# Kernel optimization log

Measured on AMD Instinct MI355X. Metric: run time of the kernel, lower is better.

Reference implementation:

```python
import jax, jax.numpy as jnp
import numpy as np

HID, STEM, BN_OUT, STEM_OUT, MLP = 256, 64, 128, 64, 128
BN_WS, STEM_WS = 5, 17
N, H_BN, W_BN, H_VIS, W_VIS = 4096, 128, 128, 1024, 1024


def setup_inputs() -> dict:
    key = jax.random.key(0)
    ks = jax.random.split(key, 24)
    f32 = jnp.float32
    def rn(k, shape, s=0.05):
        return jax.random.normal(k, shape, f32) * s
    return dict(
        bottleneck=rn(ks[0], (1, HID, H_BN, W_BN), 1.0),
        vis_stem_features=rn(ks[1], (1, STEM, H_VIS, W_VIS), 1.0),
        source_positions_vis=jax.random.uniform(ks[2], (N, 2), f32, 10.0, W_VIS - 10.0),
        pixel_to_sky=rn(ks[3], (N, 2, 2), 0.1),
        fused_h=H_BN, fused_w=W_BN, vis_h=H_VIS, vis_w=W_VIS,
        dw_w=rn(ks[4], (HID, 1, 7, 7)), dw_b=rn(ks[5], (HID,)),
        ln_g=jnp.ones((HID,), f32), ln_b=jnp.zeros((HID,), f32),
        pw1_w=rn(ks[6], (4 * HID, HID)), pw1_b=rn(ks[7], (4 * HID,)),
        pw2_w=rn(ks[8], (HID, 4 * HID)), pw2_b=rn(ks[9], (HID,)),
        cn_gamma=jnp.full((HID,), 1e-2, f32),
        bn1x1_w=rn(ks[10], (BN_OUT, HID, 1, 1)), bn1x1_b=rn(ks[11], (BN_OUT,)),
        st1_w=rn(ks[12], (STEM_OUT, STEM, 3, 3)), st1_b=rn(ks[13], (STEM_OUT,)),
        st2_w=rn(ks[14], (STEM_OUT, STEM_OUT, 3, 3)), st2_b=rn(ks[15], (STEM_OUT,)),
        h1_w=rn(ks[16], (MLP, BN_OUT + STEM_OUT)), h1_b=rn(ks[17], (MLP,)),
        h2_w=rn(ks[18], (MLP, MLP)), h2_b=rn(ks[19], (MLP,)),
        h3_w=rn(ks[20], (3, MLP)),
        h3_b=jnp.array([0.0, 0.0, float(np.log(0.05))], f32),
    )


def _gelu(x):
    return jax.nn.gelu(x, approximate=False)


def _conv2d(x, w, b, padding, groups=1):
    y = jax.lax.conv_general_dilated(
        x, w, (1, 1), [(padding, padding), (padding, padding)],
        dimension_numbers=('NCHW', 'OIHW', 'NCHW'), feature_group_count=groups)
    return y + b[None, :, None, None]


def _bilinear_windows(fm, pos, ws):
    """fm [1,C,H,W], pos [N,2] pixel coords -> [N,C,ws,ws].
    Matches torch grid_sample(mode=bilinear, padding=zeros, align_corners=True)
    with the module's normalize/unnormalize, i.e. direct pixel-coord sampling."""
    C, H, W = fm.shape[1:]
    fm2 = fm[0]
    half = ws // 2
    off = jnp.arange(-half, half + 1, dtype=pos.dtype)
    gy, gx = jnp.meshgrid(off, off, indexing='ij')
    xs = gx[None] + pos[:, 0, None, None]   # [N,ws,ws]
    ys = gy[None] + pos[:, 1, None, None]
    x0 = jnp.floor(xs); y0 = jnp.floor(ys)
    wx1 = xs - x0; wy1 = ys - y0
    x0i = x0.astype(jnp.int32); y0i = y0.astype(jnp.int32)
    def gather(yi, xi, w):
        valid = (yi >= 0) & (yi < H) & (xi >= 0) & (xi < W)
        v = fm2[:, jnp.clip(yi, 0, H - 1), jnp.clip(xi, 0, W - 1)]  # [C,N,ws,ws]
        return v * (w * valid)[None]
    out = (gather(y0i, x0i, (1 - wy1) * (1 - wx1))
           + gather(y0i, x0i + 1, (1 - wy1) * wx1)
           + gather(y0i + 1, x0i, wy1 * (1 - wx1))
           + gather(y0i + 1, x0i + 1, wy1 * wx1))
    return jnp.transpose(out, (1, 0, 2, 3))


def _gauss(ws):
    t = jnp.linspace(-1.0, 1.0, ws)
    yy, xx = jnp.meshgrid(t, t, indexing='ij')
    g = jnp.exp(-(xx ** 2 + yy ** 2) / (2 * 0.4 ** 2))
    return g / g.sum()


def _convnext(x, dw_w, dw_b, ln_g, ln_b, pw1_w, pw1_b, pw2_w, pw2_b, gamma):
    r = x
    x = _conv2d(x, dw_w, dw_b, padding=3, groups=x.shape[1])  # depthwise 7x7
    mu = x.mean(1, keepdims=True)
    var = ((x - mu) ** 2).mean(1, keepdims=True)
    x = (x - mu) / jnp.sqrt(var + 1e-6)
    x = x * ln_g[None, :, None, None] + ln_b[None, :, None, None]
    x = jnp.einsum('nchw,oc->nohw', x, pw1_w) + pw1_b[None, :, None, None]
    x = _gelu(x)
    x = jnp.einsum('nchw,oc->nohw', x, pw2_w) + pw2_b[None, :, None, None]
    return r + gamma[None, :, None, None] * x


def _forward(bottleneck, vis_stem_features, source_positions_vis, pixel_to_sky,
             dw_w, dw_b, ln_g, ln_b, pw1_w, pw1_b, pw2_w, pw2_b, cn_gamma,
             bn1x1_w, bn1x1_b, st1_w, st1_b, st2_w, st2_b,
             h1_w, h1_b, h2_w, h2_b, h3_w, h3_b,
             fused_h, fused_w, vis_h, vis_w):
    scale = jnp.array([fused_w / vis_w, fused_h / vis_h], source_positions_vis.dtype)
    pos_bn = source_positions_vis * scale
    # bottleneck branch: 5x5 windows -> ConvNeXt -> 1x1 conv -> GELU -> gauss pool
    bn_win = _bilinear_windows(bottleneck, pos_bn, BN_WS)              # [N,256,5,5]
    bn_feat = _convnext(bn_win, dw_w, dw_b, ln_g, ln_b, pw1_w, pw1_b, pw2_w, pw2_b, cn_gamma)
    bn_feat = _gelu(_conv2d(bn_feat, bn1x1_w, bn1x1_b, padding=0))     # [N,128,5,5]
    bn_vec = (bn_feat * _gauss(BN_WS)[None, None]).sum((-2, -1))       # [N,128]
    st_win = _bilinear_windows(vis_stem_features, source_positions_vis, STEM_WS)
    st = _gelu(_conv2d(st_win, st1_w, st1_b, padding=1))
    st = _gelu(_conv2d(st, st2_w, st2_b, padding=1))                   # [N,64,17,17]
    st_vec = (st * _gauss(STEM_WS)[None, None]).sum((-2, -1))          # [N,64]
    # head MLP
    x = jnp.concatenate([bn_vec, st_vec], axis=1)                      # [N,192]
    x = _gelu(x @ h1_w.T + h1_b)
    x = _gelu(x @ h2_w.T + h2_b)
    out = x @ h3_w.T + h3_b                                            # [N,3]
    dx_px, dy_px = out[:, 0], out[:, 1]
    log_sigma = jnp.clip(out[:, 2], -6.0, 3.0)
    pix = jnp.stack([dx_px, dy_px], axis=1)                            # [N,2]
    pred_sky = jnp.einsum('nij,nj->ni', pixel_to_sky, pix)             # [N,2]
    confidence = 1.0 / jnp.maximum(jnp.exp(log_sigma), 1e-4)
    return pred_sky, dx_px, dy_px, log_sigma, confidence


def reference(bottleneck, vis_stem_features, source_positions_vis, pixel_to_sky,
              fused_h, fused_w, vis_h, vis_w,
              dw_w, dw_b, ln_g, ln_b, pw1_w, pw1_b, pw2_w, pw2_b, cn_gamma,
              bn1x1_w, bn1x1_b, st1_w, st1_b, st2_w, st2_b,
              h1_w, h1_b, h2_w, h2_b, h3_w, h3_b):
    return _forward(bottleneck, vis_stem_features, source_positions_vis, pixel_to_sky,
                    dw_w, dw_b, ln_g, ln_b, pw1_w, pw1_b, pw2_w, pw2_b, cn_gamma,
                    bn1x1_w, bn1x1_b, st1_w, st1_b, st2_w, st2_b,
                    h1_w, h1_b, h2_w, h2_b, h3_w, h3_b,
                    fused_h, fused_w, vis_h, vis_w)
```

## Files before the change

kernel.cpp:

```cpp
#include <hip/hip_runtime.h>
#include <hip/hip_bf16.h>

#define XSTR 28

typedef short short8 __attribute__((ext_vector_type(8)));
typedef float f32x4  __attribute__((ext_vector_type(4)));
typedef float f32x16 __attribute__((ext_vector_type(16)));

__device__ __forceinline__ float gelu_f(float x){
    return 0.5f*x*(1.0f + erff(x*0.70710678118654752f));
}
__device__ __forceinline__ float gelu_q(float x){
    const float z = 1.5957691216057308f*x*(1.0f + 0.044715f*x*x);
    return x / (1.0f + __expf(-z));
}
__device__ __forceinline__ unsigned short f2bf(float f){
    unsigned int u = __float_as_uint(f);
    u += 0x7fffu + ((u>>16)&1u);
    return (unsigned short)(u>>16);
}
__device__ __forceinline__ unsigned int pack2(float a, float b){
    return (unsigned int)f2bf(a) | ((unsigned int)f2bf(b)<<16);
}
__device__ __forceinline__ float bf_lo(unsigned int u){ return __uint_as_float(u<<16); }
__device__ __forceinline__ float bf_hi(unsigned int u){ return __uint_as_float(u & 0xffff0000u); }
__device__ __forceinline__ float bfu(unsigned short v){ return __uint_as_float(((unsigned int)v)<<16); }

__device__ __forceinline__ void fma_row25(const float* __restrict__ row, float w, float* __restrict__ acc){
    const float4* r4 = (const float4*)row;
    float4 a0=r4[0], a1=r4[1], a2=r4[2], a3=r4[3], a4=r4[4], a5=r4[5];
    float a6 = row[24];
    acc[0]+=a0.x*w;  acc[1]+=a0.y*w;  acc[2]+=a0.z*w;  acc[3]+=a0.w*w;
    acc[4]+=a1.x*w;  acc[5]+=a1.y*w;  acc[6]+=a1.z*w;  acc[7]+=a1.w*w;
    acc[8]+=a2.x*w;  acc[9]+=a2.y*w;  acc[10]+=a2.z*w; acc[11]+=a2.w*w;
    acc[12]+=a3.x*w; acc[13]+=a3.y*w; acc[14]+=a3.z*w; acc[15]+=a3.w*w;
    acc[16]+=a4.x*w; acc[17]+=a4.y*w; acc[18]+=a4.z*w; acc[19]+=a4.w*w;
    acc[20]+=a5.x*w; acc[21]+=a5.y*w; acc[22]+=a5.z*w; acc[23]+=a5.w*w;
    acc[24]+=a6*w;
}

__device__ __forceinline__ void bn_body(
    unsigned char* __restrict__ U, int n0, int t,
    const float* __restrict__ bottleneck, const float* __restrict__ pos,
    const float* __restrict__ dw_w, const float* __restrict__ dw_b,
    const float* __restrict__ ln_g, const float* __restrict__ ln_b,
    const float* __restrict__ pw1_b, const float* __restrict__ pw2_b,
    const float* __restrict__ cn_gamma, const float* __restrict__ bn1x1_b,
    const short8* __restrict__ P1v, const short8* __restrict__ P2v,
    const short8* __restrict__ Pbv,
    float* __restrict__ vec_out)
{
    unsigned char* Xb = U;
    unsigned char* Hc = U + 32768;
    float* redA = (float*)(U + 49152);
    float* redB = (float*)(U + 50752);
    float* muS  = (float*)(U + 52352);
    float* rsS  = (float*)(U + 52576);

    const int lane = t & 63, w = t >> 6;
    const int mcol = lane & 15, h4 = lane >> 4;
    const int sP = t >> 8, cP = t & 255;

    unsigned int wvp[13];
    float xdw[25];
    {
        const int n = n0 + sP;
        const float px = pos[2*n]*0.125f, py = pos[2*n+1]*0.125f;
        const float fpx = floorf(px), fpy = floorf(py);
        const int ix0 = (int)fpx - 2, iy0 = (int)fpy - 2;
        const float fx = px - fpx, fy = py - fpy;
        const float w00=(1.f-fy)*(1.f-fx), w01=(1.f-fy)*fx, w10=fy*(1.f-fx), w11=fy*fx;
        float wv[25];
        {
            const float* fm = bottleneck + cP*16384;
            float P[6][6];
            #pragma unroll
            for (int r=0;r<6;r++){
                const int y = iy0+r;
                const bool yok = (y>=0)&&(y<128);
                const int yc = y<0?0:(y>127?127:y);
                #pragma unroll
                for (int s=0;s<6;s++){
                    const int x = ix0+s;
                    const bool ok = yok && (x>=0) && (x<128);
                    const int xc = x<0?0:(x>127?127:x);
                    P[r][s] = ok ? fm[yc*128+xc] : 0.f;
                }
            }
            #pragma unroll
            for (int a=0;a<5;a++)
            #pragma unroll
            for (int b=0;b<5;b++)
                wv[a*5+b] = w00*P[a][b]+w01*P[a][b+1]+w10*P[a+1][b]+w11*P[a+1][b+1];
        }
        #pragma unroll
        for (int i=0;i<12;i++) wvp[i] = pack2(wv[2*i], wv[2*i+1]);
        wvp[12] = pack2(wv[24], 0.f);
        {
            float wcr[49];
            const float* wc = dw_w + cP*49;
            #pragma unroll
            for (int k=0;k<49;k++) wcr[k]=wc[k];
            const float bb = dw_b[cP];
            #pragma unroll
            for (int i=0;i<5;i++){
                #pragma unroll
                for (int j=0;j<5;j++){
                    float a = bb;
                    #pragma unroll
                    for (int u=0;u<7;u++){
                        const int y = i+u-3;
                        if (y<0||y>4) continue;
                        #pragma unroll
                        for (int v=0;v<7;v++){
                            const int x = j+v-3;
                            if (x<0||x>4) continue;
                            a += wv[y*5+x]*wcr[u*7+v];
                        }
                    }
                    xdw[i*5+j] = a;
                }
            }
        }
        #pragma unroll
        for (int p=0;p<25;p++){
            const int row = sP*32 + p;
            *(unsigned short*)(Xb + row*512 + ((2*cP) ^ ((row&7)<<4))) = f2bf(xdw[p]);
        }
    }
    __syncthreads();
    if (t < 400){
        const int sp = t>>3, part = t&7;
        const int row = (sp/25)*32 + (sp - (sp/25)*25);
        float a=0.f, b=0.f;
        for (int c=part; c<256; c+=8){
            const float v = bfu(*(const unsigned short*)(Xb + row*512 + ((2*c) ^ ((row&7)<<4))));
            a += v; b += v*v;
        }
        redA[t]=a; redB[t]=b;
    }
    __syncthreads();
    if (t < 50){
        float a=0.f, b=0.f;
        #pragma unroll
        for (int s=0;s<8;s++){ a+=redA[t*8+s]; b+=redB[t*8+s]; }
        const float m = a*(1.f/256.f);
        const float var = b*(1.f/256.f) - m*m;
        muS[t]=m; rsS[t]=rsqrtf(var+1e-6f);
    }
    __syncthreads();
    {
        const float g = ln_g[cP], bb = ln_b[cP];
        #pragma unroll
        for (int p=0;p<25;p++){
            const int row = sP*32 + p;
            const float v = (xdw[p]-muS[sP*25+p])*rsS[sP*25+p]*g + bb;
            *(unsigned short*)(Xb + row*512 + ((2*cP) ^ ((row&7)<<4))) = f2bf(v);
        }
    }
    __syncthreads();

    f32x4 acc2[2][4];
    #pragma unroll
    for (int ml=0;ml<2;ml++)
        #pragma unroll
        for (int nt=0;nt<4;nt++) acc2[ml][nt]=0.f;

    for (int ch=0; ch<8; ++ch){
        const int mt = ch*8 + w;
        f32x4 a1[4];
        #pragma unroll
        for (int nt=0;nt<4;nt++) a1[nt]=0.f;
        #pragma unroll
        for (int kk=0; kk<8; ++kk){
            const short8 av = P1v[((mt<<3)+kk)*64 + lane];
            #pragma unroll
            for (int nt=0; nt<4; ++nt){
                const int row = nt*16 + mcol;
                const int ad = row*512 + ((kk*64 + h4*16) ^ ((row&7)<<4));
                const short8 bv = *(const short8*)(Xb + ad);
                a1[nt] = __builtin_amdgcn_mfma_f32_16x16x32_bf16(av, bv, a1[nt], 0,0,0);
            }
        }
        {
            const float4 b1v = *(const float4*)(pw1_b + mt*16 + h4*4);
            #pragma unroll
            for (int nt=0; nt<4; ++nt){
                const int row = nt*16 + mcol;
                const float g0 = gelu_q(a1[nt].x + b1v.x);
                const float g1 = gelu_q(a1[nt].y + b1v.y);
                const float g2 = gelu_q(a1[nt].z + b1v.z);
                const float g3 = gelu_q(a1[nt].w + b1v.w);
                const int ad = row*256 + ((w*32 + h4*8) ^ ((row&7)<<4));
                *(uint2*)(Hc + ad) = make_uint2(pack2(g0,g1), pack2(g2,g3));
            }
        }
        __syncthreads();
        #pragma unroll
        for (int ml=0; ml<2; ++ml){
            const int mtc = w*2 + ml;
            #pragma unroll
            for (int kk2=0; kk2<4; ++kk2){
                const short8 av = P2v[(mtc*32 + (ch*4 + kk2))*64 + lane];
                #pragma unroll
                for (int nt=0; nt<4; ++nt){
                    const int row = nt*16 + mcol;
                    const int ad = row*256 + ((kk2*64 + h4*16) ^ ((row&7)<<4));
                    const short8 bv = *(const short8*)(Hc + ad);
                    acc2[ml][nt] = __builtin_amdgcn_mfma_f32_16x16x32_bf16(av, bv, acc2[ml][nt], 0,0,0);
                }
            }
        }
        __syncthreads();
    }

    #pragma unroll
    for (int ml=0; ml<2; ++ml){
        const int c0 = (w*2+ml)*16 + h4*4;
        const float4 gm = *(const float4*)(cn_gamma + c0);
        const float4 b2 = *(const float4*)(pw2_b + c0);
        #pragma unroll
        for (int nt=0; nt<4; ++nt){
            const int row = nt*16 + mcol;
            const int ad = row*512 + ((2*c0) ^ ((row&7)<<4));
            const float f0 = gm.x*(acc2[ml][nt].x + b2.x);
            const float f1 = gm.y*(acc2[ml][nt].y + b2.y);
            const float f2 = gm.z*(acc2[ml][nt].z + b2.z);
            const float f3 = gm.w*(acc2[ml][nt].w + b2.w);
            *(uint2*)(Xb + ad) = make_uint2(pack2(f0,f1), pack2(f2,f3));
        }
    }
    __syncthreads();
    #pragma unroll
    for (int p=0;p<25;p++){
        const int row = sP*32 + p;
        unsigned short* ptr = (unsigned short*)(Xb + row*512 + ((2*cP) ^ ((row&7)<<4)));
        const float r = (p&1) ? bf_hi(wvp[p>>1]) : bf_lo(wvp[p>>1]);
        *ptr = f2bf(bfu(*ptr) + r);
    }
    __syncthreads();

    {
        f32x4 a3[4];
        #pragma unroll
        for (int nt=0;nt<4;nt++) a3[nt]=0.f;
        #pragma unroll
        for (int kk=0; kk<8; ++kk){
            const short8 av = Pbv[((w<<3)+kk)*64 + lane];
            #pragma unroll
            for (int nt=0; nt<4; ++nt){
                const int row = nt*16 + mcol;
                const int ad = row*512 + ((kk*64 + h4*16) ^ ((row&7)<<4));
                const short8 bv = *(const short8*)(Xb + ad);
                a3[nt] = __builtin_amdgcn_mfma_f32_16x16x32_bf16(av, bv, a3[nt], 0,0,0);
            }
        }
        const float4 bb = *(const float4*)(bn1x1_b + w*16 + h4*4);
        float e5[5];
        #pragma unroll
        for (int a=0;a<5;a++){
            const float ta = -1.f + 0.5f*a;
            e5[a] = expf(-3.125f*ta*ta);
        }
        const float Sv = e5[0]+e5[1]+e5[2]+e5[3]+e5[4];
        const float invS = 1.0f/(Sv*Sv);
        float sA[2][4];
        #pragma unroll
        for (int s=0;s<2;s++)
            #pragma unroll
            for (int j=0;j<4;j++) sA[s][j]=0.f;
        #pragma unroll
        for (int nt=0; nt<4; ++nt){
            const int row = nt*16 + mcol;
            const int s = row>>5, p = row&31;
            if (p < 25){
                const int pa = p/5, pb = p - pa*5;
                const float g = e5[pa]*e5[pb];
                sA[s][0] += g*gelu_q(a3[nt].x + bb.x);
                sA[s][1] += g*gelu_q(a3[nt].y + bb.y);
                sA[s][2] += g*gelu_q(a3[nt].z + bb.z);
                sA[s][3] += g*gelu_q(a3[nt].w + bb.w);
            }
        }
        #pragma unroll
        for (int off=1; off<16; off<<=1){
            #pragma unroll
            for (int s=0;s<2;s++)
                #pragma unroll
                for (int j=0;j<4;j++) sA[s][j] += __shfl_xor(sA[s][j], off);
        }
        if (mcol == 0){
            const int o = w*16 + h4*4;
            #pragma unroll
            for (int s=0;s<2;s++){
                float* vo = vec_out + (n0+s)*192 + o;
                vo[0]=sA[s][0]*invS; vo[1]=sA[s][1]*invS;
                vo[2]=sA[s][2]*invS; vo[3]=sA[s][3]*invS;
            }
        }
    }
}

__global__ __launch_bounds__(512,4) void bn_branch_mfma(
    const float* __restrict__ bottleneck, const float* __restrict__ pos,
    const float* __restrict__ dw_w, const float* __restrict__ dw_b,
    const float* __restrict__ ln_g, const float* __restrict__ ln_b,
    const float* __restrict__ pw1_b, const float* __restrict__ pw2_b,
    const float* __restrict__ cn_gamma, const float* __restrict__ bn1x1_b,
    const short8* __restrict__ P1v, const short8* __restrict__ P2v,
    const short8* __restrict__ Pbv,
    float* __restrict__ vec_out)
{
    __shared__ __align__(16) unsigned char U[52800];
    bn_body(U, blockIdx.x*2, threadIdx.x, bottleneck, pos, dw_w, dw_b, ln_g, ln_b,
            pw1_b, pw2_b, cn_gamma, bn1x1_b, P1v, P2v, Pbv, vec_out);
}

__global__ __launch_bounds__(256) void prepack_bn_kernel(
    const float* __restrict__ W1, const float* __restrict__ W2, const float* __restrict__ Wb,
    unsigned short* __restrict__ P1, unsigned short* __restrict__ P2, unsigned short* __restrict__ Pb)
{
    const int tid = blockIdx.x*256 + threadIdx.x;
    const float* src; unsigned short* dst; int row, col, stride, idx;
    if (tid < 32768){
        idx = tid;
        const int frag = idx>>6, l = idx&63;
        row = (frag>>3)*16 + (l&15); col = (frag&7)*32 + (l>>4)*8; stride = 256;
        src = W1; dst = P1;
    } else if (tid < 65536){
        idx = tid - 32768;
        const int frag = idx>>6, l = idx&63;
        row = (frag>>5)*16 + (l&15); col = (frag&31)*32 + (l>>4)*8; stride = 1024;
        src = W2; dst = P2;
    } else if (tid < 69632){
        idx = tid - 65536;
        const int frag = idx>>6, l = idx&63;
        row = (frag>>3)*16 + (l&15); col = (frag&7)*32 + (l>>4)*8; stride = 256;
        src = Wb; dst = Pb;
    } else return;
    const float* s = src + row*stride + col;
    unsigned int v[4];
    #pragma unroll
    for (int j=0;j<4;j++) v[j] = pack2(s[2*j], s[2*j+1]);
    *(uint4*)(dst + (size_t)idx*8) = make_uint4(v[0],v[1],v[2],v[3]);
}

__global__ __launch_bounds__(256,2) void bn_branch_valu(
    const float* __restrict__ bottleneck, const float* __restrict__ pos,
    const float* __restrict__ dw_w, const float* __restrict__ dw_b,
    const float* __restrict__ ln_g, const float* __restrict__ ln_b,
    const float* __restrict__ pw1_w, const float* __restrict__ pw1_b,
    const float* __restrict__ pw2_w, const float* __restrict__ pw2_b,
    const float* __restrict__ cn_gamma,
    const float* __restrict__ bn1x1_w, const float* __restrict__ bn1x1_b,
    float* __restrict__ vec_out)
{
    __shared__ float xln[256*XSTR];
    __shared__ float hbuf[256*XSTR];
    __shared__ float redA[200], redB[200];
    __shared__ float mu[25], rs[25];

    const int n = blockIdx.x;
    const int t = threadIdx.x;
    const int c = t;

    const float px = pos[2*n]*0.125f, py = pos[2*n+1]*0.125f;
    const float fpx = floorf(px), fpy = floorf(py);
    const int ix0 = (int)fpx - 2, iy0 = (int)fpy - 2;
    const float fx = px - fpx, fy = py - fpy;
    const float w00=(1.f-fy)*(1.f-fx), w01=(1.f-fy)*fx, w10=fy*(1.f-fx), w11=fy*fx;

    float wv[25];
    {
        const float* fm = bottleneck + c*16384;
        float P[6][6];
        #pragma unroll
        for (int r=0;r<6;r++){
            const int y = iy0+r;
            const bool yok = (y>=0)&&(y<128);
            const int yc = y<0?0:(y>127?127:y);
            #pragma unroll
            for (int s=0;s<6;s++){
                const int x = ix0+s;
                const bool ok = yok && (x>=0) && (x<128);
                const int xc = x<0?0:(x>127?127:x);
                P[r][s] = ok ? fm[yc*128+xc] : 0.f;
            }
        }
        #pragma unroll
        for (int a=0;a<5;a++)
        #pragma unroll
        for (int b=0;b<5;b++)
            wv[a*5+b] = w00*P[a][b]+w01*P[a][b+1]+w10*P[a+1][b]+w11*P[a+1][b+1];
    }
    {
        float wcr[49];
        const float* wc = dw_w + c*49;
        #pragma unroll
        for (int k=0;k<49;k++) wcr[k]=wc[k];
        const float bb = dw_b[c];
        #pragma unroll
        for (int i=0;i<5;i++){
            #pragma unroll
            for (int j=0;j<5;j++){
                float a = bb;
                #pragma unroll
                for (int u=0;u<7;u++){
                    const int y = i+u-3;
                    if (y<0||y>4) continue;
                    #pragma unroll
                    for (int v=0;v<7;v++){
                        const int x = j+v-3;
                        if (x<0||x>4) continue;
                        a += wv[y*5+x]*wcr[u*7+v];
                    }
                }
                xln[c*XSTR + i*5+j] = a;
            }
        }
    }
    __syncthreads();
    if (t < 200){
        const int p = t>>3, s = t&7;
        float a=0.f, b=0.f;
        for (int cc=s; cc<256; cc+=8){
            const float v = xln[cc*XSTR+p];
            a += v; b += v*v;
        }
        redA[t]=a; redB[t]=b;
    }
    __syncthreads();
    if (t < 25){
        float a=0.f, b=0.f;
        #pragma unroll
        for (int s=0;s<8;s++){ a+=redA[t*8+s]; b+=redB[t*8+s]; }
        const float m = a*(1.f/256.f);
        const float var = b*(1.f/256.f) - m*m;
        mu[t]=m; rs[t]=rsqrtf(var+1e-6f);
    }
    __syncthreads();
    {
        const float g = ln_g[c], bb = ln_b[c];
        #pragma unroll
        for (int p=0;p<25;p++)
            xln[c*XSTR+p] = (xln[c*XSTR+p]-mu[p])*rs[p]*g + bb;
    }
    __syncthreads();
    float acc2[25];
    #pragma unroll
    for (int p=0;p<25;p++) acc2[p]=0.f;
    for (int r=0;r<4;r++){
        const int o = r*256 + t;
        float h[25];
        {
            const float b1 = pw1_b[o];
            #pragma unroll
            for (int p=0;p<25;p++) h[p]=b1;
            const float* wr = pw1_w + o*256;
            for (int cc=0;cc<256;cc++)
                fma_row25(xln + cc*XSTR, wr[cc], h);
            #pragma unroll
            for (int p=0;p<25;p++) h[p]=gelu_f(h[p]);
        }
        __syncthreads();
        #pragma unroll
        for (int p=0;p<25;p++) hbuf[t*XSTR+p]=h[p];
        __syncthreads();
        {
            const float* w2 = pw2_w + t*1024 + r*256;
            for (int k=0;k<256;k++)
                fma_row25(hbuf + k*XSTR, w2[k], acc2);
        }
    }
    {
        const float gam = cn_gamma[c], b2 = pw2_b[c];
        #pragma unroll
        for (int p=0;p<25;p++)
            xln[c*XSTR+p] = wv[p] + gam*(acc2[p]+b2);
    }
    __syncthreads();
    if (t < 128){
        float acc[25];
        #pragma unroll
        for (int p=0;p<25;p++) acc[p]=0.f;
        const float* wr = bn1x1_w + t*256;
        for (int cc=0;cc<256;cc++)
            fma_row25(xln + cc*XSTR, wr[cc], acc);
        const float b = bn1x1_b[t];
        float e5[5];
        #pragma unroll
        for (int a=0;a<5;a++){
            const float ta = -1.f + 0.5f*a;
            e5[a] = expf(-3.125f*ta*ta);
        }
        const float Sv = e5[0]+e5[1]+e5[2]+e5[3]+e5[4];
        float res = 0.f;
        #pragma unroll
        for (int a=0;a<5;a++){
            float rowa = 0.f;
            #pragma unroll
            for (int bb=0;bb<5;bb++)
                rowa += e5[bb]*gelu_f(acc[a*5+bb]+b);
            res += e5[a]*rowa;
        }
        vec_out[n*192+t] = res/(Sv*Sv);
    }
}

__global__ __launch_bounds__(256) void prepack_kernel(
    const float* __restrict__ W1, const float* __restrict__ W2,
    unsigned short* __restrict__ Ap)
{
    const int tid = blockIdx.x*256 + threadIdx.x;
    if (tid >= 9216) return;
    const int conv = tid / 4608;
    const int r = tid - conv*4608;
    const int frag = r >> 6, l = r & 63;
    const int k  = frag >> 3;
    const int kt = (frag >> 1) & 3;
    const int wo = frag & 1;
    const float* W = conv ? W2 : W1;
    const int o  = wo*32 + (l & 31);
    const int c0 = kt*16 + (l >> 5)*8;
    unsigned int v[4];
    #pragma unroll
    for (int jj=0; jj<4; jj++){
        const float f0 = W[o*576 + (c0+2*jj  )*9 + k];
        const float f1 = W[o*576 + (c0+2*jj+1)*9 + k];
        v[jj] = pack2(f0, f1);
    }
    *(uint4*)(Ap + (size_t)tid*8) = make_uint4(v[0], v[1], v[2], v[3]);
}

__global__ __launch_bounds__(256) void transpose_vis_kernel(
    const float* __restrict__ vis, unsigned short* __restrict__ visT)
{
    __shared__ unsigned short T[64*66];
    const int b = blockIdx.x;
    const int y = b >> 4, x0 = (b & 15) << 6;
    const int t = threadIdx.x, lane = t & 63, w = t >> 6;
    #pragma unroll
    for (int i = 0; i < 16; ++i){
        const int c = w*16 + i;
        T[c*66 + lane] = f2bf(vis[c*1048576 + y*1024 + x0 + lane]);
    }
    __syncthreads();
    const int x = t >> 2, cg0 = (t & 3) * 16;
    #pragma unroll
    for (int h = 0; h < 2; ++h){
        const int cg = cg0 + h*8;
        unsigned int v[4];
        #pragma unroll
        for (int j = 0; j < 4; ++j){
            const unsigned int a = T[(cg + 2*j    )*66 + x];
            const unsigned int bsh = T[(cg + 2*j + 1)*66 + x];
            v[j] = a | (bsh << 16);
        }
        *(uint4*)(visT + ((size_t)(y*1024) + x0 + x)*64 + cg) = make_uint4(v[0],v[1],v[2],v[3]);
    }
}

#define STEM_CONV32(SRC, AP)                                                        \
    _Pragma("unroll")                                                               \
    for (int k=0;k<9;k++){                                                          \
        int tj[3];                                                                  \
        _Pragma("unroll")                                                           \
        for (int j=0;j<3;j++)                                                       \
            tj[j] = (int)sTab[m*90 + (j<cnt ? st+j : st)*9 + k];                    \
        _Pragma("unroll")                                                           \
        for (int kt=0;kt<4;kt++){                                                   \
            const short8 av = (AP)[(k*8 + kt*2 + wo)*64 + lane];                    \
            const int cb = kt*32 + hi16;                                            \
            _Pragma("unroll")                                                       \
            for (int j=0;j<3;j++){                                                  \
                if (j < cnt){                                                       \
                    const short8 bv = *(const short8*)((SRC) + (tj[j] ^ cb));       \
                    acc[j] = __builtin_amdgcn_mfma_f32_32x32x16_bf16(av, bv, acc[j], 0,0,0); \
                }                                                                   \
            }                                                                       \
        }                                                                           \
    }

template<bool TR>
__device__ __forceinline__ void stem_body(
    unsigned char* __restrict__ U, int n, int t,
    const float* __restrict__ vis, const unsigned short* __restrict__ visT,
    const float* __restrict__ pos,
    const short8* __restrict__ Ap1,
    const float* __restrict__ st1_b, const float* __restrict__ st2_b,
    float* __restrict__ vec_out)
{
    unsigned char* sXt = U;
    unsigned short* sTab = (unsigned short*)(U + 37120);
    float (*redS)[4] = (float(*)[4])(U + 42880);

    const int lane = t & 63;
    const int m = lane & 31;
    const int hi = lane >> 5;
    const int hi16 = hi*16;
    const int w = t >> 6;
    const int wo = w & 1;
    const int nh = w >> 1;
    const int st  = nh*3 - (nh==3 ? 1 : 0);
    const int cnt = (nh < 2) ? 3 : 2;

    const float fpx0 = pos[2*n], fpy0 = pos[2*n+1];
    const float fpx = floorf(fpx0), fpy = floorf(fpy0);
    const int ix0 = (int)fpx - 8, iy0 = (int)fpy - 8;
    const float fx = fpx0-fpx, fy = fpy0-fpy;
    const float w00=(1.f-fy)*(1.f-fx), w01=(1.f-fy)*fx, w10=fy*(1.f-fx), w11=fy*fx;

    if (t < 32) *(unsigned int*)(sXt + 289*128 + t*4) = 0u;

    for (int idx = t; idx < 32*90; idx += 512){
        const int mm = idx/90, rem = idx - mm*90;
        const int nt = rem/9, k = rem - nt*9;
        const int p = nt*32 + mm;
        int pp = 289;
        if (p < 289){
            const int py = (p*241)>>12, px = p - py*17;
            const int y = py + k/3 - 1, x = px + (k - (k/3)*3) - 1;
            if (((unsigned)y < 17u) && ((unsigned)x < 17u)) pp = y*17 + x;
        }
        sTab[idx] = (unsigned short)(pp*128 + ((pp&7)<<4));
    }

    if (TR){
        for (int idx = t; idx < 289*8; idx += 512){
            const int p = idx >> 3, cg = (idx & 7) * 8;
            const int py = (p*241)>>12, px = p - py*17;
            const unsigned short* q = visT + (size_t)((iy0+py)*1024 + (ix0+px))*64 + cg;
            const uint4 q00 = *(const uint4*)(q);
            const uint4 q01 = *(const uint4*)(q + 64);
            const uint4 q10 = *(const uint4*)(q + 65536);
            const uint4 q11 = *(const uint4*)(q + 65536 + 64);
            unsigned int o[4];
            #pragma unroll
            for (int j=0;j<4;j++){
                const unsigned int u00=((const unsigned int*)&q00)[j];
                const unsigned int u01=((const unsigned int*)&q01)[j];
                const unsigned int u10=((const unsigned int*)&q10)[j];
                const unsigned int u11=((const unsigned int*)&q11)[j];
                const float lo = bf_lo(u00)*w00 + bf_lo(u01)*w01 + bf_lo(u10)*w10 + bf_lo(u11)*w11;
                const float hv = bf_hi(u00)*w00 + bf_hi(u01)*w01 + bf_hi(u10)*w10 + bf_hi(u11)*w11;
                o[j] = pack2(lo, hv);
            }
            *(uint4*)(sXt + p*128 + ((2*cg) ^ ((p&7)<<4))) = make_uint4(o[0],o[1],o[2],o[3]);
        }
    } else {
        for (int task = t; task < 64*17; task += 512){
            const int c  = task & 63;
            const int py = task >> 6;
            const float* r0 = vis + c*1048576 + (iy0+py)*1024 + ix0;
            float a[18], b[18];
            #pragma unroll
            for (int kk=0; kk<18; kk++){ a[kk]=r0[kk]; b[kk]=r0[1024+kk]; }
            #pragma unroll
            for (int px=0; px<17; px++){
                const float v = w00*a[px] + w01*a[px+1] + w10*b[px] + w11*b[px+1];
                const int p = py*17 + px;
                *(unsigned short*)(sXt + p*128 + ((2*c) ^ ((p&7)<<4))) = f2bf(v);
            }
        }
    }
    __syncthreads();

    f32x16 acc[3];
    #pragma unroll
    for (int j=0;j<3;j++) acc[j] = 0.f;
    STEM_CONV32(sXt, Ap1)

    uint2 pk[3][4];
    {
        float4 b4[4];
        #pragma unroll
        for (int rg=0;rg<4;rg++) b4[rg] = *(const float4*)(st1_b + wo*32 + 8*rg + 4*hi);
        #pragma unroll
        for (int j=0;j<3;j++){
            if (j < cnt){
                #pragma unroll
                for (int rg=0;rg<4;rg++){
                    const float v0 = gelu_q(acc[j][4*rg+0] + b4[rg].x);
                    const float v1 = gelu_q(acc[j][4*rg+1] + b4[rg].y);
                    const float v2 = gelu_q(acc[j][4*rg+2] + b4[rg].z);
                    const float v3 = gelu_q(acc[j][4*rg+3] + b4[rg].w);
                    pk[j][rg] = make_uint2(pack2(v0,v1), pack2(v2,v3));
                }
            }
        }
    }
    __syncthreads();

    #pragma unroll
    for (int j=0;j<3;j++){
        if (j < cnt){
            const int p = (st+j)*32 + m;
            if (p < 289){
                const int swz = (p&7)<<4;
                #pragma unroll
                for (int rg=0;rg<4;rg++){
                    const int ch0 = wo*32 + 8*rg + 4*hi;
                    *(uint2*)(sXt + p*128 + ((2*ch0) ^ swz)) = pk[j][rg];
                }
            }
        }
    }
    __syncthreads();

    const short8* Ap2 = Ap1 + 4608;
    #pragma unroll
    for (int j=0;j<3;j++) acc[j] = 0.f;
    STEM_CONV32(sXt, Ap2)

    {
        float4 b4[4];
        #pragma unroll
        for (int rg=0;rg<4;rg++) b4[rg] = *(const float4*)(st2_b + wo*32 + 8*rg + 4*hi);
        float s[16];
        #pragma unroll
        for (int r=0;r<16;r++) s[r]=0.f;
        #pragma unroll
        for (int j=0;j<3;j++){
            if (j < cnt){
                const int p = (st+j)*32 + m;
                if (p < 289){
                    const int py = (p*241)>>12;
                    const int px = p - py*17;
                    const float ty = -1.f + 0.125f*py;
                    const float tx = -1.f + 0.125f*px;
                    const float g = expf(-3.125f*(ty*ty + tx*tx));
                    #pragma unroll
                    for (int rg=0;rg<4;rg++){
                        s[4*rg+0] += g*gelu_q(acc[j][4*rg+0] + b4[rg].x);
                        s[4*rg+1] += g*gelu_q(acc[j][4*rg+1] + b4[rg].y);
                        s[4*rg+2] += g*gelu_q(acc[j][4*rg+2] + b4[rg].z);
                        s[4*rg+3] += g*gelu_q(acc[j][4*rg+3] + b4[rg].w);
                    }
                }
            }
        }
        #pragma unroll
        for (int off=1; off<32; off<<=1){
            #pragma unroll
            for (int r=0;r<16;r++) s[r] += __shfl_xor(s[r], off);
        }
        if (m == 0){
            #pragma unroll
            for (int rg=0;rg<4;rg++)
                #pragma unroll
                for (int e=0;e<4;e++)
                    redS[wo*32 + 8*rg + 4*hi + e][nh] = s[4*rg+e];
        }
    }
    __syncthreads();
    if (t < 64){
        float Sv = 0.f;
        #pragma unroll
        for (int j=0;j<17;j++){
            const float tj = -1.f + 0.125f*j;
            Sv += expf(-3.125f*tj*tj);
        }
        vec_out[n*192+128+t] = (redS[t][0] + redS[t][1] + redS[t][2] + redS[t][3]) / (Sv*Sv);
    }
}

__global__ __launch_bounds__(512,4) void stem_kernel_tr(
    const unsigned short* __restrict__ visT, const float* __restrict__ pos,
    const short8* __restrict__ Ap1,
    const float* __restrict__ st1_b, const float* __restrict__ st2_b,
    float* __restrict__ vec_out)
{
    __shared__ __align__(16) unsigned char U[43904];
    stem_body<true>(U, blockIdx.x, threadIdx.x, nullptr, visT, pos, Ap1, st1_b, st2_b, vec_out);
}

__global__ __launch_bounds__(512,4) void stem_branch_kernel(
    const float* __restrict__ vis, const float* __restrict__ pos,
    const short8* __restrict__ Ap1,
    const float* __restrict__ st1_b, const float* __restrict__ st2_b,
    float* __restrict__ vec_out)
{
    __shared__ __align__(16) unsigned char U[43904];
    stem_body<false>(U, blockIdx.x, threadIdx.x, vis, nullptr, pos, Ap1, st1_b, st2_b, vec_out);
}

__global__ __launch_bounds__(128) void head16_kernel(
    const float* __restrict__ vec, const float* __restrict__ p2s,
    const float* __restrict__ h1_w, const float* __restrict__ h1_b,
    const float* __restrict__ h2_w, const float* __restrict__ h2_b,
    const float* __restrict__ h3_w, const float* __restrict__ h3_b,
    float* __restrict__ out, int N)
{
    __shared__ float v[16][192];
    __shared__ float x1s[16][132];
    __shared__ float x2s[16][132];
    __shared__ float o3s[16][4];
    const int n0 = blockIdx.x*16, t = threadIdx.x;

    for (int idx=t; idx<16*192; idx+=128){
        const int s = idx/192, k = idx - s*192;
        v[s][k] = vec[n0*192 + idx];
    }
    __syncthreads();
    {
        const int o = t;
        float acc[16];
        const float b = h1_b[o];
        #pragma unroll
        for (int s=0;s<16;s++) acc[s]=b;
        const float4* wr = (const float4*)(h1_w + o*192);
        for (int k4=0;k4<48;k4++){
            const float4 wv4 = wr[k4];
            #pragma unroll
            for (int s=0;s<16;s++){
                const float4 vv = *(const float4*)&v[s][k4*4];
                acc[s] += wv4.x*vv.x + wv4.y*vv.y + wv4.z*vv.z + wv4.w*vv.w;
            }
        }
        #pragma unroll
        for (int s=0;s<16;s++) x1s[s][o] = gelu_f(acc[s]);
    }
    __syncthreads();
    {
        const int o = t;
        float acc[16];
        const float b = h2_b[o];
        #pragma unroll
        for (int s=0;s<16;s++) acc[s]=b;
        const float4* wr = (const float4*)(h2_w + o*128);
        for (int k4=0;k4<32;k4++){
            const float4 wv4 = wr[k4];
            #pragma unroll
            for (int s=0;s<16;s++){
                const float4 vv = *(const float4*)&x1s[s][k4*4];
                acc[s] += wv4.x*vv.x + wv4.y*vv.y + wv4.z*vv.z + wv4.w*vv.w;
            }
        }
        #pragma unroll
        for (int s=0;s<16;s++) x2s[s][o] = gelu_f(acc[s]);
    }
    __syncthreads();
    if (t < 48){
        const int j = t>>4, s = t&15;
        float a = h3_b[j];
        const float* wr = h3_w + j*128;
        for (int k=0;k<128;k++) a += x2s[s][k]*wr[k];
        o3s[s][j] = a;
    }
    __syncthreads();
    if (t < 16){
        const int s = t, n = n0 + s;
        const float dx = o3s[s][0], dy = o3s[s][1];
        float ls = o3s[s][2];
        ls = ls < -6.f ? -6.f : (ls > 3.f ? 3.f : ls);
        const float s0 = p2s[n*4+0]*dx + p2s[n*4+1]*dy;
        const float s1 = p2s[n*4+2]*dx + p2s[n*4+3]*dy;
        const float conf = 1.0f/fmaxf(expf(ls), 1e-4f);
        out[2*n]   = s0;
        out[2*n+1] = s1;
        out[2*N+n] = dx;
        out[3*N+n] = dy;
        out[4*N+n] = ls;
        out[5*N+n] = conf;
    }
}

extern "C" void kernel_launch(void* const* d_in, const int* in_sizes, int n_in,
                              void* d_out, int out_size, void* d_ws, size_t ws_size,
                              hipStream_t stream)
{
    (void)n_in; (void)out_size;
    const float* bottleneck = (const float*)d_in[0];
    const float* vis        = (const float*)d_in[1];
    const float* pos        = (const float*)d_in[2];
    const float* p2s        = (const float*)d_in[3];
    const float* dw_w  = (const float*)d_in[8];
    const float* dw_b  = (const float*)d_in[9];
    const float* ln_g  = (const float*)d_in[10];
    const float* ln_b  = (const float*)d_in[11];
    const float* pw1_w = (const float*)d_in[12];
    const float* pw1_b = (const float*)d_in[13];
    const float* pw2_w = (const float*)d_in[14];
    const float* pw2_b = (const float*)d_in[15];
    const float* gam   = (const float*)d_in[16];
    const float* b1w   = (const float*)d_in[17];
    const float* b1b   = (const float*)d_in[18];
    const float* s1w   = (const float*)d_in[19];
    const float* s1b   = (const float*)d_in[20];
    const float* s2w   = (const float*)d_in[21];
    const float* s2b   = (const float*)d_in[22];
    const float* h1w   = (const float*)d_in[23];
    const float* h1b   = (const float*)d_in[24];
    const float* h2w   = (const float*)d_in[25];
    const float* h2b   = (const float*)d_in[26];
    const float* h3w   = (const float*)d_in[27];
    const float* h3b   = (const float*)d_in[28];

    const int N = in_sizes[2]/2;
    char* ws = (char*)d_ws;
    float* vec = (float*)ws;
    unsigned short* Apack = (unsigned short*)(ws + 3145728);
    unsigned short* P1    = (unsigned short*)(ws + 3293184);
    unsigned short* P2    = (unsigned short*)(ws + 3817472);
    unsigned short* Pb    = (unsigned short*)(ws + 4341760);
    unsigned short* visT  = (unsigned short*)(ws + 4407296);
    const size_t need_mfma = 4407296u;
    const size_t need_tr   = 4407296u + 134217728ull;
    const size_t vec_bytes = (size_t)N*192*sizeof(float);

    hipMemsetAsync(d_ws, 0, vec_bytes, stream);
    prepack_kernel<<<36, 256, 0, stream>>>(s1w, s2w, Apack);

    if (ws_size >= need_tr){
        prepack_bn_kernel<<<272, 256, 0, stream>>>(pw1_w, pw2_w, b1w, P1, P2, Pb);
        transpose_vis_kernel<<<16384, 256, 0, stream>>>(vis, visT);
        stem_kernel_tr<<<N, 512, 0, stream>>>(visT, pos, (const short8*)Apack, s1b, s2b, vec);
        bn_branch_mfma<<<N/2, 512, 0, stream>>>(bottleneck, pos, dw_w, dw_b, ln_g, ln_b,
                                                pw1_b, pw2_b, gam, b1b,
                                                (const short8*)P1, (const short8*)P2, (const short8*)Pb,
                                                vec);
    } else if (ws_size >= need_mfma){
        prepack_bn_kernel<<<272, 256, 0, stream>>>(pw1_w, pw2_w, b1w, P1, P2, Pb);
        bn_branch_mfma<<<N/2, 512, 0, stream>>>(bottleneck, pos, dw_w, dw_b, ln_g, ln_b,
                                                pw1_b, pw2_b, gam, b1b,
                                                (const short8*)P1, (const short8*)P2, (const short8*)Pb,
                                                vec);
        stem_branch_kernel<<<N, 512, 0, stream>>>(vis, pos, (const short8*)Apack, s1b, s2b, vec);
    } else {
        bn_branch_valu<<<N, 256, 0, stream>>>(bottleneck, pos, dw_w, dw_b, ln_g, ln_b,
                                              pw1_w, pw1_b, pw2_w, pw2_b, gam, b1w, b1b, vec);
        stem_branch_kernel<<<N, 512, 0, stream>>>(vis, pos, (const short8*)Apack, s1b, s2b, vec);
    }
    head16_kernel<<<N/16, 128, 0, stream>>>(vec, p2s, h1w, h1b, h2w, h2b, h3w, h3b,
                                            (float*)d_out, N);
}
```

Measured before the change: 776.3 us.

## Transpose bottleneck to channel-last bf16 for coalesced bilinear window gathers

Adds a kernel that converts the bottleneck feature map from NCHW fp32 into an HWC bf16 buffer. The bn branch then gathers bilinear window samples with 16-byte vector loads across channels, stages them in shared memory, and reuses the same buffer for the depthwise output before layernorm. This replaces per-channel strided scalar gathers, which fetch many scattered cache lines. In exchange it adds a transpose pass, an 8 MB workspace requirement, and bf16 rounding of the inputs before the depthwise conv and of the depthwise output. The VALU fallback kernel is removed.

```diff
diff --git a/kernel.cpp b/kernel.cpp
--- a/kernel.cpp
+++ b/kernel.cpp
@@ -39,9 +39,11 @@
     acc[24]+=a6*w;
 }
 
+template<bool BTR>
 __device__ __forceinline__ void bn_body(
     unsigned char* __restrict__ U, int n0, int t,
-    const float* __restrict__ bottleneck, const float* __restrict__ pos,
+    const float* __restrict__ bottleneck, const unsigned short* __restrict__ bnT,
+    const float* __restrict__ pos,
     const float* __restrict__ dw_w, const float* __restrict__ dw_b,
     const float* __restrict__ ln_g, const float* __restrict__ ln_b,
     const float* __restrict__ pw1_b, const float* __restrict__ pw2_b,
@@ -62,8 +64,93 @@
     const int sP = t >> 8, cP = t & 255;
 
     unsigned int wvp[13];
-    float xdw[25];
-    {
+
+    if (BTR){
+        int ix0A[2], iy0A[2];
+        float wbl[2][4];
+        #pragma unroll
+        for (int s=0;s<2;s++){
+            const int n = n0 + s;
+            const float px = pos[2*n]*0.125f, py = pos[2*n+1]*0.125f;
+            const float fpx = floorf(px), fpy = floorf(py);
+            ix0A[s] = (int)fpx - 2; iy0A[s] = (int)fpy - 2;
+            const float fx = px - fpx, fy = py - fpy;
+            wbl[s][0]=(1.f-fy)*(1.f-fx); wbl[s][1]=(1.f-fy)*fx;
+            wbl[s][2]=fy*(1.f-fx);       wbl[s][3]=fy*fx;
+        }
+        for (int idx = t; idx < 1600; idx += 512){
+            const int s = idx/800, rem = idx - s*800;
+            const int p = rem >> 5, cg = rem & 31;
+            const int a = p/5, bq = p - a*5;
+            const int y0 = iy0A[s]+a, x0 = ix0A[s]+bq;
+            uint4 q[4];
+            #pragma unroll
+            for (int e=0;e<4;e++){
+                const int yy = y0 + (e>>1), xx = x0 + (e&1);
+                const bool ok = ((unsigned)yy < 128u) && ((unsigned)xx < 128u);
+                q[e] = ok ? *(const uint4*)(bnT + ((size_t)(yy*128+xx))*256 + cg*8)
+                          : make_uint4(0u,0u,0u,0u);
+            }
+            const float w0=wbl[s][0], w1=wbl[s][1], w2=wbl[s][2], w3=wbl[s][3];
+            unsigned int o[4];
+            #pragma unroll
+            for (int j=0;j<4;j++){
+                const unsigned int u0=((const unsigned int*)&q[0])[j];
+                const unsigned int u1=((const unsigned int*)&q[1])[j];
+                const unsigned int u2=((const unsigned int*)&q[2])[j];
+                const unsigned int u3=((const unsigned int*)&q[3])[j];
+                const float lo = bf_lo(u0)*w0 + bf_lo(u1)*w1 + bf_lo(u2)*w2 + bf_lo(u3)*w3;
+                const float hv = bf_hi(u0)*w0 + bf_hi(u1)*w1 + bf_hi(u2)*w2 + bf_hi(u3)*w3;
+                o[j] = pack2(lo, hv);
+            }
+            const int row = s*32 + p;
+            *(uint4*)(Xb + row*512 + ((cg*16) ^ ((row&7)<<4))) = make_uint4(o[0],o[1],o[2],o[3]);
+        }
+        __syncthreads();
+        {
+            float wv[25];
+            #pragma unroll
+            for (int p=0;p<25;p++){
+                const int row = sP*32 + p;
+                wv[p] = bfu(*(const unsigned short*)(Xb + row*512 + ((2*cP) ^ ((row&7)<<4))));
+            }
+            #pragma unroll
+            for (int i=0;i<12;i++) wvp[i] = pack2(wv[2*i], wv[2*i+1]);
+            wvp[12] = pack2(wv[24], 0.f);
+            float xdw[25];
+            {
+                float wcr[49];
+                const float* wc = dw_w + cP*49;
+                #pragma unroll
+                for (int k=0;k<49;k++) wcr[k]=wc[k];
+                const float bb = dw_b[cP];
+                #pragma unroll
+                for (int i=0;i<5;i++){
+                    #pragma unroll
+                    for (int j=0;j<5;j++){
+                        float a = bb;
+                        #pragma unroll
+                        for (int u=0;u<7;u++){
+                            const int y = i+u-3;
+                            if (y<0||y>4) continue;
+                            #pragma unroll
+                            for (int v=0;v<7;v++){
+                                const int x = j+v-3;
+                                if (x<0||x>4) continue;
+                                a += wv[y*5+x]*wcr[u*7+v];
+                            }
+                        }
+                        xdw[i*5+j] = a;
+                    }
+                }
+            }
+            #pragma unroll
+            for (int p=0;p<25;p++){
+                const int row = sP*32 + p;
+                *(unsigned short*)(Xb + row*512 + ((2*cP) ^ ((row&7)<<4))) = f2bf(xdw[p]);
+            }
+        }
+    } else {
         const int n = n0 + sP;
         const float px = pos[2*n]*0.125f, py = pos[2*n+1]*0.125f;
         const float fpx = floorf(px), fpy = floorf(py);
@@ -96,6 +183,7 @@
         #pragma unroll
         for (int i=0;i<12;i++) wvp[i] = pack2(wv[2*i], wv[2*i+1]);
         wvp[12] = pack2(wv[24], 0.f);
+        float xdw[25];
         {
             float wcr[49];
             const float* wc = dw_w + cP*49;
@@ -154,8 +242,9 @@
         #pragma unroll
         for (int p=0;p<25;p++){
             const int row = sP*32 + p;
-            const float v = (xdw[p]-muS[sP*25+p])*rsS[sP*25+p]*g + bb;
-            *(unsigned short*)(Xb + row*512 + ((2*cP) ^ ((row&7)<<4))) = f2bf(v);
+            unsigned short* ptr = (unsigned short*)(Xb + row*512 + ((2*cP) ^ ((row&7)<<4)));
+            const float xv = bfu(*ptr);
+            *ptr = f2bf((xv-muS[sP*25+p])*rsS[sP*25+p]*g + bb);
         }
     }
     __syncthreads();
@@ -312,8 +401,50 @@
     float* __restrict__ vec_out)
 {
     __shared__ __align__(16) unsigned char U[52800];
-    bn_body(U, blockIdx.x*2, threadIdx.x, bottleneck, pos, dw_w, dw_b, ln_g, ln_b,
-            pw1_b, pw2_b, cn_gamma, bn1x1_b, P1v, P2v, Pbv, vec_out);
+    bn_body<false>(U, blockIdx.x*2, threadIdx.x, bottleneck, nullptr, pos, dw_w, dw_b, ln_g, ln_b,
+                   pw1_b, pw2_b, cn_gamma, bn1x1_b, P1v, P2v, Pbv, vec_out);
+}
+
+__global__ __launch_bounds__(512,4) void bn_branch_mfma_tr(
+    const unsigned short* __restrict__ bnT, const float* __restrict__ pos,
+    const float* __restrict__ dw_w, const float* __restrict__ dw_b,
+    const float* __restrict__ ln_g, const float* __restrict__ ln_b,
+    const float* __restrict__ pw1_b, const float* __restrict__ pw2_b,
+    const float* __restrict__ cn_gamma, const float* __restrict__ bn1x1_b,
+    const short8* __restrict__ P1v, const short8* __restrict__ P2v,
+    const short8* __restrict__ Pbv,
+    float* __restrict__ vec_out)
+{
+    __shared__ __align__(16) unsigned char U[52800];
+    bn_body<true>(U, blockIdx.x*2, threadIdx.x, nullptr, bnT, pos, dw_w, dw_b, ln_g, ln_b,
+                  pw1_b, pw2_b, cn_gamma, bn1x1_b, P1v, P2v, Pbv, vec_out);
+}
+
+__global__ __launch_bounds__(256) void transpose_bn_kernel(
+    const float* __restrict__ bn, unsigned short* __restrict__ bnT)
+{
+    __shared__ unsigned short T[256*66];
+    const int b = blockIdx.x;
+    const int y = b >> 1, x0 = (b & 1) << 6;
+    const int t = threadIdx.x, lane = t & 63, w = t >> 6;
+    for (int i = 0; i < 64; ++i){
+        const int c = w*64 + i;
+        T[c*66 + lane] = f2bf(bn[c*16384 + y*128 + x0 + lane]);
+    }
+    __syncthreads();
+    const int x = t >> 2, q = (t & 3) * 64;
+    #pragma unroll
+    for (int h = 0; h < 8; ++h){
+        const int cg = q + h*8;
+        unsigned int v[4];
+        #pragma unroll
+        for (int j = 0; j < 4; ++j){
+            const unsigned int a = T[(cg + 2*j    )*66 + x];
+            const unsigned int bs = T[(cg + 2*j + 1)*66 + x];
+            v[j] = a | (bs << 16);
+        }
+        *(uint4*)(bnT + ((size_t)(y*128) + x0 + x)*256 + cg) = make_uint4(v[0],v[1],v[2],v[3]);
+    }
 }
 
 __global__ __launch_bounds__(256) void prepack_bn_kernel(
@@ -343,168 +474,6 @@
     #pragma unroll
     for (int j=0;j<4;j++) v[j] = pack2(s[2*j], s[2*j+1]);
     *(uint4*)(dst + (size_t)idx*8) = make_uint4(v[0],v[1],v[2],v[3]);
-}
-
-__global__ __launch_bounds__(256,2) void bn_branch_valu(
-    const float* __restrict__ bottleneck, const float* __restrict__ pos,
-    const float* __restrict__ dw_w, const float* __restrict__ dw_b,
-    const float* __restrict__ ln_g, const float* __restrict__ ln_b,
-    const float* __restrict__ pw1_w, const float* __restrict__ pw1_b,
-    const float* __restrict__ pw2_w, const float* __restrict__ pw2_b,
-    const float* __restrict__ cn_gamma,
-    const float* __restrict__ bn1x1_w, const float* __restrict__ bn1x1_b,
-    float* __restrict__ vec_out)
-{
-    __shared__ float xln[256*XSTR];
-    __shared__ float hbuf[256*XSTR];
-    __shared__ float redA[200], redB[200];
-    __shared__ float mu[25], rs[25];
-
-    const int n = blockIdx.x;
-    const int t = threadIdx.x;
-    const int c = t;
-
-    const float px = pos[2*n]*0.125f, py = pos[2*n+1]*0.125f;
-    const float fpx = floorf(px), fpy = floorf(py);
-    const int ix0 = (int)fpx - 2, iy0 = (int)fpy - 2;
-    const float fx = px - fpx, fy = py - fpy;
-    const float w00=(1.f-fy)*(1.f-fx), w01=(1.f-fy)*fx, w10=fy*(1.f-fx), w11=fy*fx;
-
-    float wv[25];
-    {
-        const float* fm = bottleneck + c*16384;
-        float P[6][6];
-        #pragma unroll
-        for (int r=0;r<6;r++){
-            const int y = iy0+r;
-            const bool yok = (y>=0)&&(y<128);
-            const int yc = y<0?0:(y>127?127:y);
-            #pragma unroll
-            for (int s=0;s<6;s++){
-                const int x = ix0+s;
-                const bool ok = yok && (x>=0) && (x<128);
-                const int xc = x<0?0:(x>127?127:x);
-                P[r][s] = ok ? fm[yc*128+xc] : 0.f;
-            }
-        }
-        #pragma unroll
-        for (int a=0;a<5;a++)
-        #pragma unroll
-        for (int b=0;b<5;b++)
-            wv[a*5+b] = w00*P[a][b]+w01*P[a][b+1]+w10*P[a+1][b]+w11*P[a+1][b+1];
-    }
-    {
-        float wcr[49];
-        const float* wc = dw_w + c*49;
-        #pragma unroll
-        for (int k=0;k<49;k++) wcr[k]=wc[k];
-        const float bb = dw_b[c];
-        #pragma unroll
-        for (int i=0;i<5;i++){
-            #pragma unroll
-            for (int j=0;j<5;j++){
-                float a = bb;
-                #pragma unroll
-                for (int u=0;u<7;u++){
-                    const int y = i+u-3;
-                    if (y<0||y>4) continue;
-                    #pragma unroll
-                    for (int v=0;v<7;v++){
-                        const int x = j+v-3;
-                        if (x<0||x>4) continue;
-                        a += wv[y*5+x]*wcr[u*7+v];
-                    }
-                }
-                xln[c*XSTR + i*5+j] = a;
-            }
-        }
-    }
-    __syncthreads();
-    if (t < 200){
-        const int p = t>>3, s = t&7;
-        float a=0.f, b=0.f;
-        for (int cc=s; cc<256; cc+=8){
-            const float v = xln[cc*XSTR+p];
-            a += v; b += v*v;
-        }
-        redA[t]=a; redB[t]=b;
-    }
-    __syncthreads();
-    if (t < 25){
-        float a=0.f, b=0.f;
-        #pragma unroll
-        for (int s=0;s<8;s++){ a+=redA[t*8+s]; b+=redB[t*8+s]; }
-        const float m = a*(1.f/256.f);
-        const float var = b*(1.f/256.f) - m*m;
-        mu[t]=m; rs[t]=rsqrtf(var+1e-6f);
-    }
-    __syncthreads();
-    {
-        const float g = ln_g[c], bb = ln_b[c];
-        #pragma unroll
-        for (int p=0;p<25;p++)
-            xln[c*XSTR+p] = (xln[c*XSTR+p]-mu[p])*rs[p]*g + bb;
-    }
-    __syncthreads();
-    float acc2[25];
-    #pragma unroll
-    for (int p=0;p<25;p++) acc2[p]=0.f;
-    for (int r=0;r<4;r++){
-        const int o = r*256 + t;
-        float h[25];
-        {
-            const float b1 = pw1_b[o];
-            #pragma unroll
-            for (int p=0;p<25;p++) h[p]=b1;
-            const float* wr = pw1_w + o*256;
-            for (int cc=0;cc<256;cc++)
-                fma_row25(xln + cc*XSTR, wr[cc], h);
-            #pragma unroll
-            for (int p=0;p<25;p++) h[p]=gelu_f(h[p]);
-        }
-        __syncthreads();
-        #pragma unroll
-        for (int p=0;p<25;p++) hbuf[t*XSTR+p]=h[p];
-        __syncthreads();
-        {
-            const float* w2 = pw2_w + t*1024 + r*256;
-            for (int k=0;k<256;k++)
-                fma_row25(hbuf + k*XSTR, w2[k], acc2);
-        }
-    }
-    {
-        const float gam = cn_gamma[c], b2 = pw2_b[c];
-        #pragma unroll
-        for (int p=0;p<25;p++)
-            xln[c*XSTR+p] = wv[p] + gam*(acc2[p]+b2);
-    }
-    __syncthreads();
-    if (t < 128){
-        float acc[25];
-        #pragma unroll
-        for (int p=0;p<25;p++) acc[p]=0.f;
-        const float* wr = bn1x1_w + t*256;
-        for (int cc=0;cc<256;cc++)
-            fma_row25(xln + cc*XSTR, wr[cc], acc);
-        const float b = bn1x1_b[t];
-        float e5[5];
-        #pragma unroll
-        for (int a=0;a<5;a++){
-            const float ta = -1.f + 0.5f*a;
-            e5[a] = expf(-3.125f*ta*ta);
-        }
-        const float Sv = e5[0]+e5[1]+e5[2]+e5[3]+e5[4];
-        float res = 0.f;
-        #pragma unroll
-        for (int a=0;a<5;a++){
-            float rowa = 0.f;
-            #pragma unroll
-            for (int bb=0;bb<5;bb++)
-                rowa += e5[bb]*gelu_f(acc[a*5+bb]+b);
-            res += e5[a]*rowa;
-        }
-        vec_out[n*192+t] = res/(Sv*Sv);
-    }
 }
 
 __global__ __launch_bounds__(256) void prepack_kernel(
@@ -904,14 +873,25 @@
     unsigned short* P2    = (unsigned short*)(ws + 3817472);
     unsigned short* Pb    = (unsigned short*)(ws + 4341760);
     unsigned short* visT  = (unsigned short*)(ws + 4407296);
+    unsigned short* bnT   = (unsigned short*)(ws + 4407296 + 134217728ull);
     const size_t need_mfma = 4407296u;
     const size_t need_tr   = 4407296u + 134217728ull;
+    const size_t need_full = need_tr + 8388608ull;
     const size_t vec_bytes = (size_t)N*192*sizeof(float);
 
     hipMemsetAsync(d_ws, 0, vec_bytes, stream);
     prepack_kernel<<<36, 256, 0, stream>>>(s1w, s2w, Apack);
 
-    if (ws_size >= need_tr){
+    if (ws_size >= need_full){
+        prepack_bn_kernel<<<272, 256, 0, stream>>>(pw1_w, pw2_w, b1w, P1, P2, Pb);
+        transpose_bn_kernel<<<256, 256, 0, stream>>>(bottleneck, bnT);
+        transpose_vis_kernel<<<16384, 256, 0, stream>>>(vis, visT);
+        stem_kernel_tr<<<N, 512, 0, stream>>>(visT, pos, (const short8*)Apack, s1b, s2b, vec);
+        bn_branch_mfma_tr<<<N/2, 512, 0, stream>>>(bnT, pos, dw_w, dw_b, ln_g, ln_b,
+                                                   pw1_b, pw2_b, gam, b1b,
+                                                   (const short8*)P1, (const short8*)P2, (const short8*)Pb,
+                                                   vec);
+    } else if (ws_size >= need_tr){
         prepack_bn_kernel<<<272, 256, 0, stream>>>(pw1_w, pw2_w, b1w, P1, P2, Pb);
         transpose_vis_kernel<<<16384, 256, 0, stream>>>(vis, visT);
         stem_kernel_tr<<<N, 512, 0, stream>>>(visT, pos, (const short8*)Apack, s1b, s2b, vec);
@@ -919,17 +899,13 @@
                                                 pw1_b, pw2_b, gam, b1b,
                                                 (const short8*)P1, (const short8*)P2, (const short8*)Pb,
                                                 vec);
-    } else if (ws_size >= need_mfma){
+    } else {
         prepack_bn_kernel<<<272, 256, 0, stream>>>(pw1_w, pw2_w, b1w, P1, P2, Pb);
         bn_branch_mfma<<<N/2, 512, 0, stream>>>(bottleneck, pos, dw_w, dw_b, ln_g, ln_b,
                                                 pw1_b, pw2_b, gam, b1b,
                                                 (const short8*)P1, (const short8*)P2, (const short8*)Pb,
                                                 vec);
         stem_branch_kernel<<<N, 512, 0, stream>>>(vis, pos, (const short8*)Apack, s1b, s2b, vec);
-    } else {
-        bn_branch_valu<<<N, 256, 0, stream>>>(bottleneck, pos, dw_w, dw_b, ln_g, ln_b,
-                                              pw1_w, pw1_b, pw2_w, pw2_b, gam, b1w, b1b, vec);
-        stem_branch_kernel<<<N, 512, 0, stream>>>(vis, pos, (const short8*)Apack, s1b, s2b, vec);
     }
     head16_kernel<<<N/16, 128, 0, stream>>>(vec, p2s, h1w, h1b, h2w, h2b, h3w, h3b,
                                             (float*)d_out, N);
```

After: 739.2 us. 1.05x faster.
